# Optimization experiments

Measured on AMD Instinct MI355X. Metric: run time of the kernel, lower is better.

The kernel has to match this reference:

```python
import jax, jax.numpy as jnp
import numpy as np
from jax import lax

L = 25            # max_delay (250 // init_spike_step=10, odd)
SIG = 12.0        # max_delay // 2, frozen (requires_grad=False)
BN_EPS = 1e-5
EPS = 1e-7


def _dcls_kernel(W, P):
    # Gaussian interpolation of kernel_count=1 weights onto a dense kernel of size L.
    # W, P: (out, in). Returns (out, in, L).
    grid = jnp.arange(L, dtype=W.dtype) - L // 2          # (L,)
    K = jnp.exp(-0.5 * ((grid[None, None, :] - P[:, :, None]) / SIG) ** 2)
    K = K / (jnp.sum(K, axis=-1, keepdims=True) + EPS)    # normalize over kernel taps
    return W[:, :, None] * K


def _dcls_conv(x_tbc, W, P):
    # x_tbc: (T, B, Cin) -> causal dilated-kernel conv over time -> (T, B, Cout)
    kernel = _dcls_kernel(W, P)                           # (Cout, Cin, L)
    xb = jnp.transpose(x_tbc, (1, 2, 0))                  # (B, Cin, T)
    xb = jnp.pad(xb, ((0, 0), (0, 0), (L - 1, 0)))        # left (causal) padding
    y = lax.conv_general_dilated(xb, kernel, window_strides=(1,), padding='VALID',
                                 dimension_numbers=('NCH', 'OIH', 'NCH'))
    return jnp.transpose(y, (2, 0, 1))                    # (T, B, Cout)


def _bn(x_tbc, gamma, beta):
    # BatchNorm1d with step_mode='m': stats over merged (T, B) per channel.
    mean = jnp.mean(x_tbc, axis=(0, 1))
    var = jnp.var(x_tbc, axis=(0, 1))
    xhat = (x_tbc - mean) * lax.rsqrt(var + BN_EPS)
    return gamma * xhat + beta


def setup_inputs() -> dict:
    key = jax.random.key(0)
    ks = jax.random.split(key, 8)
    B, T, C = 128, 100, 700
    x = jax.random.uniform(ks[0], (B, T, C), dtype=jnp.float32)
    pmax = float(L // 2)
    W1 = jax.random.normal(ks[1], (256, 700), jnp.float32) * (1.0 / np.sqrt(700))
    P1 = jax.random.uniform(ks[2], (256, 700), jnp.float32, minval=-pmax, maxval=pmax)
    W2 = jax.random.normal(ks[3], (256, 256), jnp.float32) * (1.0 / np.sqrt(256))
    P2 = jax.random.uniform(ks[4], (256, 256), jnp.float32, minval=-pmax, maxval=pmax)
    W3 = jax.random.normal(ks[5], (20, 256), jnp.float32) * (1.0 / np.sqrt(256))
    P3 = jax.random.uniform(ks[6], (20, 256), jnp.float32, minval=-pmax, maxval=pmax)
    return {
        'x': x, 'W1': W1, 'P1': P1, 'W2': W2, 'P2': P2, 'W3': W3, 'P3': P3,
        'gamma1': jnp.ones((256,), jnp.float32), 'beta1': jnp.zeros((256,), jnp.float32),
        'gamma2': jnp.ones((256,), jnp.float32), 'beta2': jnp.zeros((256,), jnp.float32),
    }


def reference(x, W1, P1, W2, P2, W3, P3, gamma1, beta1, gamma2, beta2):
    h = jnp.transpose(x, (1, 0, 2))            # (T, B, C)
    h = _dcls_conv(h, W1, P1)                  # (T, B, 256)
    h = jax.nn.relu(_bn(h, gamma1, beta1))     # dropout = identity (eval)
    h = _dcls_conv(h, W2, P2)                  # (T, B, 256)
    h = jax.nn.relu(_bn(h, gamma2, beta2))
    h = _dcls_conv(h, W3, P3)                  # (T, B, 20)
    return jnp.sum(jax.nn.softmax(h, axis=2), axis=0)   # (B, 20)
```

## Files before the change

### kernel.cpp

```cpp
#include <hip/hip_runtime.h>
#include <stdint.h>


#define T_LEN 100
#define B_SZ  128
#define M_ROWS 12800
#define R_RANK 4
#define K_FIR 448

typedef __bf16 v8bf __attribute__((ext_vector_type(8)));
typedef float  v4f  __attribute__((ext_vector_type(4)));
typedef unsigned int uint32;
typedef unsigned short ushort_t;

struct PhiT { float v[25][R_RANK]; };
constexpr double cexp_(double x) {
  double s = 1.0, t = 1.0;
  for (int n = 1; n < 30; ++n) { t = t * x / n; s += t; }
  return s;
}
constexpr PhiT make_phi() {
  PhiT P{};
  for (int tau = 0; tau < 25; ++tau) {
    double u = (tau - 12) / 12.0;
    double g = cexp_(-0.5 * u * u);
    double T0 = 1.0, T1 = u;
    P.v[tau][0] = (float)(g * T0);
    P.v[tau][1] = (float)(g * T1);
    for (int r = 2; r < R_RANK; ++r) {
      double T2 = 2.0 * u * T1 - T0;
      P.v[tau][r] = (float)(g * T2);
      T0 = T1; T1 = T2;
    }
  }
  return P;
}
constexpr PhiT PHI = make_phi();

__device__ __forceinline__ void gl_lds16(const void* g, void* l) {
  __builtin_amdgcn_global_load_lds(
      (const __attribute__((address_space(1))) char*)g,
      (__attribute__((address_space(3))) char*)l, 16, 0, 0);
}

__device__ __forceinline__ void build_wr_body(
    const float* __restrict__ W, const float* __restrict__ P,
    __bf16* __restrict__ Wr, int CIN, int CINP, int COUT, int COUTP, int o) {
  for (int i = threadIdx.x; i < CINP; i += blockDim.x) {
    bool valid = (o < COUT) && (i < CIN);
    float w = valid ? W[(size_t)o * CIN + i] : 0.f;
    float p = valid ? P[(size_t)o * CIN + i] : 0.f;
    float S = 0.f;
#pragma unroll
    for (int l = 0; l < 25; ++l) {
      float d = ((float)(l - 12) - p) * (1.f / 12.f);
      S += expf(-0.5f * d * d);
    }
    float v = p * (1.f / 12.f);
    float g = w * expf(-0.5f * v * v) / (S + 1e-7f);
    float h = 0.5f * v, hh = h * h;
    float pw = 1.f;
#pragma unroll
    for (int r = 0; r < R_RANK; ++r) {
      float term = pw, sum = pw;
#pragma unroll
      for (int m = 1; m <= 6; ++m) {
        term *= hh / (float)(m * (m + r));
        sum += term;
      }
      float c = g * ((r == 0) ? 1.f : 2.f) * sum;
      Wr[((size_t)r * COUTP + o) * CINP + i] = (__bf16)c;
      pw *= h / (float)(r + 1);
    }
  }
}

__global__ void setup_all(const float* __restrict__ x,
                          const float* __restrict__ W1, const float* __restrict__ P1,
                          const float* __restrict__ W2, const float* __restrict__ P2,
                          const float* __restrict__ W3, const float* __restrict__ P3,
                          __bf16* __restrict__ Xb, __bf16* __restrict__ Wr1,
                          __bf16* __restrict__ Wr2, __bf16* __restrict__ Wr3,
                          __bf16* __restrict__ Af, float* __restrict__ stats) {
  int blk = blockIdx.x;
  if (blk < 256) { build_wr_body(W1, P1, Wr1, 700, 704, 256, 256, blk); return; }
  blk -= 256;
  if (blk < 256) { build_wr_body(W2, P2, Wr2, 256, 256, 256, 256, blk); return; }
  blk -= 256;
  if (blk < 32) { build_wr_body(W3, P3, Wr3, 256, 256, 20, 32, blk); return; }
  blk -= 32;
  if (blk < 196) {
    int idx = blk * 256 + threadIdx.x;
    if (idx < 112 * 448) {
      int t = idx / 448, k = idx - t * 448;
      float v = 0.f;
      if (t < 100 && k < 400) {
        int r = k / 100, s = k - r * 100;
        int tau = s - t + 24;
        if (tau >= 0 && tau < 25) v = PHI.v[tau][r];
      }
      Af[idx] = (__bf16)v;
    }
    return;
  }
  blk -= 196;
  if (blk < 2200) {
    int c0 = blk * 1024 + threadIdx.x;
#pragma unroll
    for (int k = 0; k < 4; ++k) {
      int c = c0 + k * 256;
      int row = c / 176, col4 = c - row * 176;
      int t = row >> 7, b = row & 127;
      uint2 pk;
      __bf16* pb = (__bf16*)&pk;
      if (col4 < 175) {
        const float* src = x + ((size_t)b * T_LEN + t) * 700 + col4 * 4;
        float4 v = *(const float4*)src;
        pb[0] = (__bf16)v.x; pb[1] = (__bf16)v.y;
        pb[2] = (__bf16)v.z; pb[3] = (__bf16)v.w;
      } else {
        pk.x = 0u; pk.y = 0u;
      }
      *(uint2*)&Xb[(size_t)row * 704 + col4 * 4] = pk;
    }
    return;
  }
  blk -= 2200;
  if (blk == 0) {
    for (int i = threadIdx.x; i < 1024; i += 256) stats[i] = 0.f;
  }
}

template <int CINP, int BLK_N, int WROWS, int WCOLS, int CO_SH>
__global__ __launch_bounds__(256, 2)
void gemm_rk64(const __bf16* __restrict__ A, const __bf16* __restrict__ Bm,
               __bf16* __restrict__ Z) {
  constexpr int COUTP = 1 << CO_SH;
  constexpr int WM = 128 / WROWS;
  constexpr int WN = BLK_N / WCOLS;
  constexpr int RM = WM / 16;
  constexpr int RN = WN / 16;
  __shared__ __align__(16) __bf16 sA[128 * 64];
  __shared__ __align__(16) __bf16 sB[BLK_N * 64];

  const int tid = threadIdx.x;
  const int w = tid >> 6, lane = tid & 63;
  const int q = lane >> 4, ln = lane & 15;
  const int wrow = w / WCOLS, wcol = w % WCOLS;
  const int srow8 = lane >> 3;
  const int s8 = lane & 7;

  const int t0 = blockIdx.x;
  const int oc = blockIdx.y * BLK_N;
  const __bf16* Abase = A + (size_t)t0 * 128 * CINP;
  const __bf16* Bbase = Bm + (size_t)oc * CINP;

  v4f acc[RM][RN];
#pragma unroll
  for (int a = 0; a < RM; ++a)
#pragma unroll
    for (int b = 0; b < RN; ++b) acc[a][b] = v4f{0.f, 0.f, 0.f, 0.f};

  for (int ic = 0; ic < CINP; ic += 64) {
    for (int j = w; j < 16; j += 4) {
      int m = j * 8 + srow8;
      int g = s8 ^ (m & 7);
      gl_lds16(Abase + (size_t)m * CINP + ic + g * 8, &sA[j * 512]);
    }
    for (int j = w; j < BLK_N / 8; j += 4) {
      int n = j * 8 + srow8;
      int g = s8 ^ (n & 7);
      gl_lds16(Bbase + (size_t)n * CINP + ic + g * 8, &sB[j * 512]);
    }
    __syncthreads();

#pragma unroll
    for (int s = 0; s < 2; ++s) {
      v8bf af[RM], bfr[RN];
#pragma unroll
      for (int a = 0; a < RM; ++a) {
        int m = wrow * WM + a * 16 + ln;
        af[a] = *(const v8bf*)&sA[m * 64 + ((((s << 2) | q) ^ (m & 7)) * 8)];
      }
#pragma unroll
      for (int b = 0; b < RN; ++b) {
        int n = wcol * WN + b * 16 + ln;
        bfr[b] = *(const v8bf*)&sB[n * 64 + ((((s << 2) | q) ^ (n & 7)) * 8)];
      }
#pragma unroll
      for (int a = 0; a < RM; ++a)
#pragma unroll
        for (int b = 0; b < RN; ++b)
          acc[a][b] = __builtin_amdgcn_mfma_f32_16x16x32_bf16(af[a], bfr[b], acc[a][b], 0, 0, 0);
    }
    __syncthreads();
  }

#pragma unroll
  for (int a = 0; a < RM; ++a) {
#pragma unroll
    for (int b = 0; b < RN; ++b) {
      int n = oc + wcol * WN + b * 16 + ln;
      int r = n >> CO_SH, o = n & (COUTP - 1);
#pragma unroll
      for (int rr = 0; rr < 4; ++rr) {
        int m = t0 * 128 + wrow * WM + a * 16 + q * 4 + rr;
        Z[((size_t)r * M_ROWS + m) * COUTP + o] = (__bf16)acc[a][b][rr];
      }
    }
  }
}

template <int COUTP, bool STATS, bool SOFTMAX>
__global__ __launch_bounds__(256, 2)
void fir_gemm64(const __bf16* __restrict__ Af, const __bf16* __restrict__ Z,
                __bf16* __restrict__ Yout, float* __restrict__ stats,
                float* __restrict__ outp, int N) {
  __shared__ __align__(16) unsigned char smem[46592];

  const int tid = threadIdx.x;
  const int w = tid >> 6, lane = tid & 63;
  const int q = lane >> 4, ln = lane & 15;
  const int srow8 = lane >> 3, s8 = lane & 7;
  const int kp = tid >> 3;
  const int noct = tid & 7;
  const int nb = blockIdx.x * 64;

  v4f acc[7];
#pragma unroll
  for (int a = 0; a < 7; ++a) acc[a] = v4f{0.f, 0.f, 0.f, 0.f};

  uint4 r0, r1;

#define SA_BUF(b) ((__bf16*)(smem + (b) * 23296))
#define SB_BUF(b) ((uint32*)(smem + (b) * 23296 + 14336))

  {
    __bf16* sA = SA_BUF(0);
    for (int j = w; j < 14; j += 4) {
      int m = j * 8 + srow8;
      int g = s8 ^ (m & 7);
      gl_lds16(Af + (size_t)m * K_FIR + 0 + g * 8, &sA[j * 512]);
    }
    const __bf16* zp = Z + (size_t)(0 + kp * 2) * N + nb + noct * 8;
    r0 = *(const uint4*)zp;
    r1 = *(const uint4*)(zp + N);
  }

  for (int i = 0; i < 7; ++i) {
    const int cb = i & 1;
    asm volatile("s_waitcnt vmcnt(0)" ::: "memory");
    {
      uint32* sBu = SB_BUF(cb);
      const ushort_t* p0 = (const ushort_t*)&r0;
      const ushort_t* p1 = (const ushort_t*)&r1;
#pragma unroll
      for (int j = 0; j < 8; ++j) {
        uint32 val = (uint32)p0[j] | ((uint32)p1[j] << 16);
        sBu[(noct * 8 + j) * 35 + kp] = val;
      }
    }
    if (i < 6) {
      int kc = (i + 1) * 64;
      __bf16* sA = SA_BUF(cb ^ 1);
      for (int j = w; j < 14; j += 4) {
        int m = j * 8 + srow8;
        int g = s8 ^ (m & 7);
        gl_lds16(Af + (size_t)m * K_FIR + kc + g * 8, &sA[j * 512]);
      }
      const __bf16* zp = Z + (size_t)(kc + kp * 2) * N + nb + noct * 8;
      r0 = *(const uint4*)zp;
      r1 = *(const uint4*)(zp + N);
    }
    asm volatile("s_waitcnt lgkmcnt(0)" ::: "memory");
    __builtin_amdgcn_s_barrier();

    {
      __bf16* sA = SA_BUF(cb);
      uint32* sBu = SB_BUF(cb);
#pragma unroll
      for (int s = 0; s < 2; ++s) {
        v8bf af[7];
#pragma unroll
        for (int a = 0; a < 7; ++a) {
          int m = a * 16 + ln;
          af[a] = *(const v8bf*)&sA[m * 64 + ((((s << 2) | q) ^ (m & 7)) * 8)];
        }
        int base = (w * 16 + ln) * 35 + s * 16 + q * 4;
        uint32 tmp[4] = {sBu[base], sBu[base + 1], sBu[base + 2], sBu[base + 3]};
        v8bf bfr = *(const v8bf*)tmp;
#pragma unroll
        for (int a = 0; a < 7; ++a)
          acc[a] = __builtin_amdgcn_mfma_f32_16x16x32_bf16(af[a], bfr, acc[a], 0, 0, 0);
      }
    }
    __builtin_amdgcn_s_barrier();
  }

  int ng = nb + w * 16 + ln;
  if (!SOFTMAX) {
    float s = 0.f, ss = 0.f;
#pragma unroll
    for (int a = 0; a < 7; ++a) {
#pragma unroll
      for (int rr = 0; rr < 4; ++rr) {
        int t = a * 16 + q * 4 + rr;
        float v = acc[a][rr];
        if (t < 100) {
          Yout[(size_t)t * N + ng] = (__bf16)v;
          s += v; ss += v * v;
        }
      }
    }
    if (STATS) {
      s += __shfl_xor(s, 16); ss += __shfl_xor(ss, 16);
      s += __shfl_xor(s, 32); ss += __shfl_xor(ss, 32);
      if (q == 0) {
        int o = ng & (COUTP - 1);
        atomicAdd(&stats[o], s);
        atomicAdd(&stats[COUTP + o], ss);
      }
    }
  } else {
    float* smx = (float*)smem;
    float* lacc = (float*)(smem + 26000);
    int col = w * 16 + ln;
#pragma unroll
    for (int a = 0; a < 7; ++a) {
#pragma unroll
      for (int rr = 0; rr < 4; ++rr) {
        int t = a * 16 + q * 4 + rr;
        if (t < 100) smx[t * 65 + col] = acc[a][rr];
      }
    }
    if (tid < 64) lacc[tid & 63] = 0.f;
    __syncthreads();
    if (tid < 200) {
      int bl = tid / 100, t = tid - bl * 100;
      const float* rr = &smx[t * 65 + bl * 32];
      float v[20], m = -1e30f;
#pragma unroll
      for (int o = 0; o < 20; ++o) { v[o] = rr[o]; m = fmaxf(m, v[o]); }
      float sum = 0.f;
#pragma unroll
      for (int o = 0; o < 20; ++o) { v[o] = expf(v[o] - m); sum += v[o]; }
      float inv = 1.f / sum;
#pragma unroll
      for (int o = 0; o < 20; ++o) atomicAdd(&lacc[bl * 20 + o], v[o] * inv);
    }
    __syncthreads();
    if (tid < 40) {
      int bl = tid / 20, o = tid - bl * 20;
      int b = (nb >> 5) + bl;
      outp[b * 20 + o] = lacc[bl * 20 + o];
    }
  }
#undef SA_BUF
#undef SB_BUF
}

__global__ __launch_bounds__(256)
void bn_apply_relu8(__bf16* __restrict__ h, const float* __restrict__ stats,
                    const float* __restrict__ gamma, const float* __restrict__ beta) {
  int idx = blockIdx.x * 256 + threadIdx.x;
  int co = (idx & 31) * 8;
  size_t row = (size_t)(idx >> 5);
  __bf16* p = h + row * 256 + co;
  uint4 raw = *(const uint4*)p;
  const ushort_t* pr = (const ushort_t*)&raw;
  uint4 outv;
  ushort_t* po = (ushort_t*)&outv;
#pragma unroll
  for (int j = 0; j < 8; ++j) {
    int c = co + j;
    float mean = stats[c] * (1.f / 12800.f);
    float var = stats[256 + c] * (1.f / 12800.f) - mean * mean;
    float inv = rsqrtf(var + 1e-5f) * gamma[c];
    uint32 u = (uint32)pr[j] << 16;
    float xv; __builtin_memcpy(&xv, &u, 4);
    float v = (xv - mean) * inv + beta[c];
    v = fmaxf(v, 0.f);
    __bf16 bv = (__bf16)v;
    po[j] = *(const ushort_t*)&bv;
  }
  *(uint4*)p = outv;
}


extern "C" void kernel_launch(void* const* d_in, const int* in_sizes, int n_in,
                              void* d_out, int out_size, void* d_ws, size_t ws_size,
                              hipStream_t stream) {
  const float* x  = (const float*)d_in[0];
  const float* W1 = (const float*)d_in[1];
  const float* P1 = (const float*)d_in[2];
  const float* W2 = (const float*)d_in[3];
  const float* P2 = (const float*)d_in[4];
  const float* W3 = (const float*)d_in[5];
  const float* P3 = (const float*)d_in[6];
  const float* g1 = (const float*)d_in[7];
  const float* b1 = (const float*)d_in[8];
  const float* g2 = (const float*)d_in[9];
  const float* b2 = (const float*)d_in[10];
  float* out = (float*)d_out;

  constexpr size_t XB_B  = (size_t)M_ROWS * 704 * 2;
  constexpr size_t Z_B   = (size_t)K_FIR * 32768 * 2;
  constexpr size_t Y12_B = (size_t)M_ROWS * 256 * 2;
  constexpr size_t W1_B  = (size_t)R_RANK * 256 * 704 * 2;
  constexpr size_t W2_B  = (size_t)R_RANK * 256 * 256 * 2;
  constexpr size_t W3_B  = (size_t)R_RANK * 32 * 256 * 2;
  constexpr size_t AF_B  = (size_t)112 * K_FIR * 2;
  constexpr size_t ST_B  = 4096;
  constexpr size_t TOTAL = XB_B + Z_B + Y12_B + W1_B + W2_B + W3_B + AF_B + ST_B;
  if (ws_size < TOTAL) return;

  char* ws = (char*)d_ws;
  size_t off = 0;
  __bf16* Xb   = (__bf16*)(ws + off); off += XB_B;
  __bf16* Zb   = (__bf16*)(ws + off); off += Z_B;
  __bf16* Yb   = (__bf16*)(ws + off); off += Y12_B;
  __bf16* Wr1  = (__bf16*)(ws + off); off += W1_B;
  __bf16* Wr2  = (__bf16*)(ws + off); off += W2_B;
  __bf16* Wr3  = (__bf16*)(ws + off); off += W3_B;
  __bf16* Afir = (__bf16*)(ws + off); off += AF_B;
  float*  stats1 = (float*)(ws + off);
  float*  stats2 = stats1 + 512;

  setup_all<<<dim3(2941), 256, 0, stream>>>(x, W1, P1, W2, P2, W3, P3,
                                            Xb, Wr1, Wr2, Wr3, Afir, stats1);

  gemm_rk64<704, 256, 2, 2, 8><<<dim3(100, 4), 256, 0, stream>>>(Xb, Wr1, Zb);
  fir_gemm64<256, true, false><<<dim3(512), 256, 0, stream>>>(
      Afir, Zb, Yb, stats1, nullptr, 32768);
  bn_apply_relu8<<<dim3(1600), 256, 0, stream>>>(Yb, stats1, g1, b1);

  gemm_rk64<256, 256, 2, 2, 8><<<dim3(100, 4), 256, 0, stream>>>(Yb, Wr2, Zb);
  fir_gemm64<256, true, false><<<dim3(512), 256, 0, stream>>>(
      Afir, Zb, Yb, stats2, nullptr, 32768);
  bn_apply_relu8<<<dim3(1600), 256, 0, stream>>>(Yb, stats2, g2, b2);

  gemm_rk64<256, 64, 2, 2, 5><<<dim3(100, 2), 256, 0, stream>>>(Yb, Wr3, Zb);
  fir_gemm64<32, false, true><<<dim3(64), 256, 0, stream>>>(
      Afir, Zb, nullptr, nullptr, out, 4096);
}
```

Before: 187.5 us.

## Double-buffer B tile in rank GEMM and skip zero-padded Z loads in FIR

The GEMM kernel now double-buffers the B (weight) tile in shared memory and prefetches the next K-slice of B while the current one is consumed. Explicit vmcnt waits and raw s_barrier replace __syncthreads, so global loads overlap with MFMA work. Separately, the FIR kernel skips global loads of Z rows beyond index 400 and substitutes zeros, avoiding reads of padding. The hand-tuned vmcnt counts depend on how many loads each thread issues, so a wrong count could create a race. The raw barriers also drop the implicit LDS waits.

After: 193.3 us. +3.1%, slower.

```diff
diff --git a/kernel.cpp b/kernel.cpp
--- a/kernel.cpp
+++ b/kernel.cpp
@@ -140,8 +140,9 @@
   constexpr int WN = BLK_N / WCOLS;
   constexpr int RM = WM / 16;
   constexpr int RN = WN / 16;
+  constexpr int NITER = CINP / 64;
   __shared__ __align__(16) __bf16 sA[128 * 64];
-  __shared__ __align__(16) __bf16 sB[BLK_N * 64];
+  __shared__ __align__(16) __bf16 sB[2][BLK_N * 64];
 
   const int tid = threadIdx.x;
   const int w = tid >> 6, lane = tid & 63;
@@ -161,19 +162,37 @@
 #pragma unroll
     for (int b = 0; b < RN; ++b) acc[a][b] = v4f{0.f, 0.f, 0.f, 0.f};
 
-  for (int ic = 0; ic < CINP; ic += 64) {
+  for (int j = w; j < BLK_N / 8; j += 4) {
+    int n = j * 8 + srow8;
+    int g = s8 ^ (n & 7);
+    gl_lds16(Bbase + (size_t)n * CINP + 0 + g * 8, &sB[0][j * 512]);
+  }
+
+  for (int i = 0; i < NITER; ++i) {
+    const int ic = i * 64;
     for (int j = w; j < 16; j += 4) {
       int m = j * 8 + srow8;
       int g = s8 ^ (m & 7);
       gl_lds16(Abase + (size_t)m * CINP + ic + g * 8, &sA[j * 512]);
     }
-    for (int j = w; j < BLK_N / 8; j += 4) {
-      int n = j * 8 + srow8;
-      int g = s8 ^ (n & 7);
-      gl_lds16(Bbase + (size_t)n * CINP + ic + g * 8, &sB[j * 512]);
-    }
-    __syncthreads();
-
+    if (i + 1 < NITER) {
+      const int icn = ic + 64;
+      for (int j = w; j < BLK_N / 8; j += 4) {
+        int n = j * 8 + srow8;
+        int g = s8 ^ (n & 7);
+        gl_lds16(Bbase + (size_t)n * CINP + icn + g * 8, &sB[(i + 1) & 1][j * 512]);
+      }
+      if constexpr (BLK_N == 256) {
+        asm volatile("s_waitcnt vmcnt(8)" ::: "memory");
+      } else {
+        asm volatile("s_waitcnt vmcnt(2)" ::: "memory");
+      }
+    } else {
+      asm volatile("s_waitcnt vmcnt(0)" ::: "memory");
+    }
+    __builtin_amdgcn_s_barrier();
+
+    const __bf16* sBc = sB[i & 1];
 #pragma unroll
     for (int s = 0; s < 2; ++s) {
       v8bf af[RM], bfr[RN];
@@ -185,7 +204,7 @@
 #pragma unroll
       for (int b = 0; b < RN; ++b) {
         int n = wcol * WN + b * 16 + ln;
-        bfr[b] = *(const v8bf*)&sB[n * 64 + ((((s << 2) | q) ^ (n & 7)) * 8)];
+        bfr[b] = *(const v8bf*)&sBc[n * 64 + ((((s << 2) | q) ^ (n & 7)) * 8)];
       }
 #pragma unroll
       for (int a = 0; a < RM; ++a)
@@ -193,7 +212,7 @@
         for (int b = 0; b < RN; ++b)
           acc[a][b] = __builtin_amdgcn_mfma_f32_16x16x32_bf16(af[a], bfr[b], acc[a][b], 0, 0, 0);
     }
-    __syncthreads();
+    __builtin_amdgcn_s_barrier();
   }
 
 #pragma unroll
@@ -268,9 +287,14 @@
         int g = s8 ^ (m & 7);
         gl_lds16(Af + (size_t)m * K_FIR + kc + g * 8, &sA[j * 512]);
       }
-      const __bf16* zp = Z + (size_t)(kc + kp * 2) * N + nb + noct * 8;
-      r0 = *(const uint4*)zp;
-      r1 = *(const uint4*)(zp + N);
+      if (kc + kp * 2 < 400) {
+        const __bf16* zp = Z + (size_t)(kc + kp * 2) * N + nb + noct * 8;
+        r0 = *(const uint4*)zp;
+        r1 = *(const uint4*)(zp + N);
+      } else {
+        r0 = uint4{0u, 0u, 0u, 0u};
+        r1 = uint4{0u, 0u, 0u, 0u};
+      }
     }
     asm volatile("s_waitcnt lgkmcnt(0)" ::: "memory");
     __builtin_amdgcn_s_barrier();
```
